# Kernel tuning notes

Measured on AMD Instinct MI355X. Metric: run time of the kernel, lower is better.

The kernel has to match this reference:

```python
import jax, jax.numpy as jnp
import numpy as np


def _pair_indices(n_beads):
    # Replicates the torch loop ordering: all pairs at offset 1, then offset 2, ...
    i_list, j_list = [], []
    for off in range(1, n_beads):
        i = np.arange(n_beads - off)
        i_list.append(i)
        j_list.append(i + off)
    return np.concatenate(i_list), np.concatenate(j_list)


def setup_inputs() -> dict:
    key = jax.random.key(0)
    data = jax.random.normal(key, (4096, 128, 3), dtype=jnp.float32)
    return {"data": data}


def _features(data):
    n = data.shape[1]
    i_idx, j_idx = _pair_indices(n)  # static numpy index arrays

    # All pairwise distances, ordered by bead offset (matches torch loop order)
    dvec = data[:, j_idx, :] - data[:, i_idx, :]          # [B, P, 3]
    distances = jnp.linalg.norm(dvec, axis=2)             # [B, P]

    # Adjacent bond vectors: x[j+1] - x[j]
    adj = data[:, 1:, :] - data[:, :-1, :]                # [B, n-1, 3]

    # Planar angles over consecutive bond-vector pairs
    a0, a1 = adj[:, : n - 2, :], adj[:, 1 : n - 1, :]
    angles = jnp.arccos(
        jnp.sum(a0 * a1, axis=2)
        / jnp.linalg.norm(a0, axis=2)
        / jnp.linalg.norm(a1, axis=2)
    )                                                     # [B, n-2]

    # Dihedrals
    cpa = jnp.cross(a0, a1, axis=2)                       # [B, n-2, 3]
    plane = jnp.cross(cpa[:, 1 : n - 2, :], adj[:, 1 : n - 2, :], axis=2)  # [B, n-3, 3]
    c0, c1 = cpa[:, : n - 3, :], cpa[:, 1 : n - 2, :]
    nc0 = jnp.linalg.norm(c0, axis=2)
    dihedral_cos = jnp.sum(c0 * c1, axis=2) / nc0 / jnp.linalg.norm(c1, axis=2)
    p0 = plane[:, : n - 3, :]
    dihedral_sin = jnp.sum(c0 * p0, axis=2) / nc0 / jnp.linalg.norm(p0, axis=2)

    return jnp.concatenate([distances, angles, dihedral_cos, dihedral_sin], axis=1)


def reference(data):
    return _features(data)
```

## Files before the change

kernel.cpp:

```cpp
#include <hip/hip_runtime.h>
#include <math.h>

constexpr int NB    = 128;
constexpr int NPAIR = NB * (NB - 1) / 2;
constexpr int NANG  = NB - 2;
constexpr int NDIH  = NB - 3;
constexpr int ROW   = NPAIR + NANG + 2 * NDIH;

__global__ __launch_bounds__(128, 8) void dist_kernel(
        const float* __restrict__ data, float* __restrict__ out) {
    __shared__ float4 s4[NB];
    const int b = blockIdx.x;
    const int t = threadIdx.x;
    const float* src = data + (size_t)b * (NB * 3);

    s4[t] = make_float4(src[3 * t], src[3 * t + 1], src[3 * t + 2], 0.0f);
    __syncthreads();

    float* orow = out + (size_t)b * ROW;

    float px[4], py[4], pz[4];
    #pragma unroll
    for (int k = 0; k < 4; ++k) {
        int idx = t - k; if (idx < 0) idx = 0;
        float4 v = s4[idx];
        px[k] = v.x; py[k] = v.y; pz[k] = v.z;
    }

    int base = 0;
    #pragma unroll 2
    for (int off = 1; off < NB; off += 4) {
        const int len = NB - off;
        int bk0 = base;
        int bk1 = bk0 + len;
        int bk2 = bk1 + len - 1;
        int bk3 = bk2 + len - 2;
        base    = bk3 + len - 3;
        if (t < len) {
            float4 pj = s4[t + off];
            float dx, dy, dz, d;
            dx = pj.x - px[0]; dy = pj.y - py[0]; dz = pj.z - pz[0];
            d = __builtin_amdgcn_sqrtf(dx*dx + dy*dy + dz*dz);
            orow[bk0 + t] = d;
            dx = pj.x - px[1]; dy = pj.y - py[1]; dz = pj.z - pz[1];
            d = __builtin_amdgcn_sqrtf(dx*dx + dy*dy + dz*dz);
            if (t >= 1) orow[bk1 + t - 1] = d;
            dx = pj.x - px[2]; dy = pj.y - py[2]; dz = pj.z - pz[2];
            d = __builtin_amdgcn_sqrtf(dx*dx + dy*dy + dz*dz);
            if (t >= 2) orow[bk2 + t - 2] = d;
            dx = pj.x - px[3]; dy = pj.y - py[3]; dz = pj.z - pz[3];
            d = __builtin_amdgcn_sqrtf(dx*dx + dy*dy + dz*dz);
            if (t >= 3) orow[bk3 + t - 3] = d;
        }
    }
}

__global__ __launch_bounds__(128) void angle_kernel(
        const float* __restrict__ data, float* __restrict__ out) {
    __shared__ float4 s4[NB];
    const int b = blockIdx.x;
    const int t = threadIdx.x;
    const float* src = data + (size_t)b * (NB * 3);

    s4[t] = make_float4(src[3 * t], src[3 * t + 1], src[3 * t + 2], 0.0f);
    __syncthreads();

    float* orow = out + (size_t)b * ROW;

    for (int v = t; v < NANG + 2 * NDIH; v += 128) {
        if (v < NANG) {
            int k = v;
            float4 p0 = s4[k], p1 = s4[k + 1], p2 = s4[k + 2];
            float a0x = p1.x - p0.x, a0y = p1.y - p0.y, a0z = p1.z - p0.z;
            float a1x = p2.x - p1.x, a1y = p2.y - p1.y, a1z = p2.z - p1.z;
            float d  = a0x * a1x + a0y * a1y + a0z * a1z;
            float r0 = rsqrtf(a0x * a0x + a0y * a0y + a0z * a0z);
            float r1 = rsqrtf(a1x * a1x + a1y * a1y + a1z * a1z);
            float c  = d * r0 * r1;
            c = fminf(1.0f, fmaxf(-1.0f, c));
            orow[NPAIR + k] = acosf(c);
        } else {
            int k = (v < NANG + NDIH) ? (v - NANG) : (v - NANG - NDIH);
            float4 p0 = s4[k], p1 = s4[k + 1], p2 = s4[k + 2], p3 = s4[k + 3];
            float e0x = p1.x - p0.x, e0y = p1.y - p0.y, e0z = p1.z - p0.z;
            float e1x = p2.x - p1.x, e1y = p2.y - p1.y, e1z = p2.z - p1.z;
            float e2x = p3.x - p2.x, e2y = p3.y - p2.y, e2z = p3.z - p2.z;
            float c0x = e0y * e1z - e0z * e1y;
            float c0y = e0z * e1x - e0x * e1z;
            float c0z = e0x * e1y - e0y * e1x;
            float c1x = e1y * e2z - e1z * e2y;
            float c1y = e1z * e2x - e1x * e2z;
            float c1z = e1x * e2y - e1y * e2x;
            float rn0 = rsqrtf(c0x * c0x + c0y * c0y + c0z * c0z);
            if (v < NANG + NDIH) {
                float d   = c0x * c1x + c0y * c1y + c0z * c1z;
                float rn1 = rsqrtf(c1x * c1x + c1y * c1y + c1z * c1z);
                orow[NPAIR + NANG + k] = d * rn0 * rn1;
            } else {
                float qx = c1y * e1z - c1z * e1y;
                float qy = c1z * e1x - c1x * e1z;
                float qz = c1x * e1y - c1y * e1x;
                float d  = c0x * qx + c0y * qy + c0z * qz;
                float rp = rsqrtf(qx * qx + qy * qy + qz * qz);
                orow[NPAIR + NANG + NDIH + k] = d * rn0 * rp;
            }
        }
    }
}

extern "C" void kernel_launch(void* const* d_in, const int* in_sizes, int n_in,
                              void* d_out, int out_size, void* d_ws, size_t ws_size,
                              hipStream_t stream) {
    const float* data = (const float*)d_in[0];
    float* out = (float*)d_out;
    const int batch = in_sizes[0] / (NB * 3);
    dist_kernel<<<batch, 128, 0, stream>>>(data, out);
    angle_kernel<<<batch, 128, 0, stream>>>(data, out);
}
```

Measured before the change: 37.20 us.

## Fuse distance and angle kernels into one persistent-style kernel over 4 batches

Merges the pairwise-distance kernel and the angle/dihedral kernel into a single launch, so the input is loaded into shared memory once per batch and one kernel launch is removed. Each block now loops over 4 batch elements strided by the grid size, with syncthreads guarding reuse of the shared buffer. The grid shrinks to a quarter of the batch count, which cuts per-block setup but reduces the number of blocks available to hide latency. The angle work now runs serially after the distance work within each block.

Result: slower. 43.15 us (+16.0%).

```diff
diff --git a/kernel.cpp b/kernel.cpp
--- a/kernel.cpp
+++ b/kernel.cpp
@@ -6,103 +6,96 @@
 constexpr int NANG  = NB - 2;
 constexpr int NDIH  = NB - 3;
 constexpr int ROW   = NPAIR + NANG + 2 * NDIH;
+constexpr int PP    = 4;
 
-__global__ __launch_bounds__(128, 8) void dist_kernel(
-        const float* __restrict__ data, float* __restrict__ out) {
+__global__ __launch_bounds__(128, 8) void protein_feat_kernel(
+        const float* __restrict__ data, float* __restrict__ out, int batch) {
     __shared__ float4 s4[NB];
-    const int b = blockIdx.x;
     const int t = threadIdx.x;
-    const float* src = data + (size_t)b * (NB * 3);
 
-    s4[t] = make_float4(src[3 * t], src[3 * t + 1], src[3 * t + 2], 0.0f);
-    __syncthreads();
+    for (int k = 0; k < PP; ++k) {
+        const int p = blockIdx.x + gridDim.x * k;
+        if (p >= batch) break;
 
-    float* orow = out + (size_t)b * ROW;
+        __syncthreads();
+        const float* src = data + (size_t)p * (NB * 3);
+        s4[t] = make_float4(src[3 * t], src[3 * t + 1], src[3 * t + 2], 0.0f);
+        __syncthreads();
 
-    float px[4], py[4], pz[4];
-    #pragma unroll
-    for (int k = 0; k < 4; ++k) {
-        int idx = t - k; if (idx < 0) idx = 0;
-        float4 v = s4[idx];
-        px[k] = v.x; py[k] = v.y; pz[k] = v.z;
-    }
+        float* orow = out + (size_t)p * ROW;
 
-    int base = 0;
-    #pragma unroll 2
-    for (int off = 1; off < NB; off += 4) {
-        const int len = NB - off;
-        int bk0 = base;
-        int bk1 = bk0 + len;
-        int bk2 = bk1 + len - 1;
-        int bk3 = bk2 + len - 2;
-        base    = bk3 + len - 3;
-        if (t < len) {
-            float4 pj = s4[t + off];
-            float dx, dy, dz, d;
-            dx = pj.x - px[0]; dy = pj.y - py[0]; dz = pj.z - pz[0];
-            d = __builtin_amdgcn_sqrtf(dx*dx + dy*dy + dz*dz);
-            orow[bk0 + t] = d;
-            dx = pj.x - px[1]; dy = pj.y - py[1]; dz = pj.z - pz[1];
-            d = __builtin_amdgcn_sqrtf(dx*dx + dy*dy + dz*dz);
-            if (t >= 1) orow[bk1 + t - 1] = d;
-            dx = pj.x - px[2]; dy = pj.y - py[2]; dz = pj.z - pz[2];
-            d = __builtin_amdgcn_sqrtf(dx*dx + dy*dy + dz*dz);
-            if (t >= 2) orow[bk2 + t - 2] = d;
-            dx = pj.x - px[3]; dy = pj.y - py[3]; dz = pj.z - pz[3];
-            d = __builtin_amdgcn_sqrtf(dx*dx + dy*dy + dz*dz);
-            if (t >= 3) orow[bk3 + t - 3] = d;
+        float px[4], py[4], pz[4];
+        #pragma unroll
+        for (int q = 0; q < 4; ++q) {
+            int idx = t - q; if (idx < 0) idx = 0;
+            float4 v = s4[idx];
+            px[q] = v.x; py[q] = v.y; pz[q] = v.z;
         }
-    }
-}
 
-__global__ __launch_bounds__(128) void angle_kernel(
-        const float* __restrict__ data, float* __restrict__ out) {
-    __shared__ float4 s4[NB];
-    const int b = blockIdx.x;
-    const int t = threadIdx.x;
-    const float* src = data + (size_t)b * (NB * 3);
+        int base = 0;
+        #pragma unroll 2
+        for (int off = 1; off < NB; off += 4) {
+            const int len = NB - off;
+            int bk0 = base;
+            int bk1 = bk0 + len;
+            int bk2 = bk1 + len - 1;
+            int bk3 = bk2 + len - 2;
+            base    = bk3 + len - 3;
+            if (t < len) {
+                float4 pj = s4[t + off];
+                float dx, dy, dz, d;
+                dx = pj.x - px[0]; dy = pj.y - py[0]; dz = pj.z - pz[0];
+                d = __builtin_amdgcn_sqrtf(dx*dx + dy*dy + dz*dz);
+                orow[bk0 + t] = d;
+                dx = pj.x - px[1]; dy = pj.y - py[1]; dz = pj.z - pz[1];
+                d = __builtin_amdgcn_sqrtf(dx*dx + dy*dy + dz*dz);
+                if (t >= 1) orow[bk1 + t - 1] = d;
+                dx = pj.x - px[2]; dy = pj.y - py[2]; dz = pj.z - pz[2];
+                d = __builtin_amdgcn_sqrtf(dx*dx + dy*dy + dz*dz);
+                if (t >= 2) orow[bk2 + t - 2] = d;
+                dx = pj.x - px[3]; dy = pj.y - py[3]; dz = pj.z - pz[3];
+                d = __builtin_amdgcn_sqrtf(dx*dx + dy*dy + dz*dz);
+                if (t >= 3) orow[bk3 + t - 3] = d;
+            }
+        }
 
-    s4[t] = make_float4(src[3 * t], src[3 * t + 1], src[3 * t + 2], 0.0f);
-    __syncthreads();
-
-    float* orow = out + (size_t)b * ROW;
-
-    for (int v = t; v < NANG + 2 * NDIH; v += 128) {
-        if (v < NANG) {
-            int k = v;
-            float4 p0 = s4[k], p1 = s4[k + 1], p2 = s4[k + 2];
-            float a0x = p1.x - p0.x, a0y = p1.y - p0.y, a0z = p1.z - p0.z;
-            float a1x = p2.x - p1.x, a1y = p2.y - p1.y, a1z = p2.z - p1.z;
-            float d  = a0x * a1x + a0y * a1y + a0z * a1z;
-            float r0 = rsqrtf(a0x * a0x + a0y * a0y + a0z * a0z);
-            float r1 = rsqrtf(a1x * a1x + a1y * a1y + a1z * a1z);
-            float c  = d * r0 * r1;
-            c = fminf(1.0f, fmaxf(-1.0f, c));
-            orow[NPAIR + k] = acosf(c);
-        } else {
-            int k = (v < NANG + NDIH) ? (v - NANG) : (v - NANG - NDIH);
-            float4 p0 = s4[k], p1 = s4[k + 1], p2 = s4[k + 2], p3 = s4[k + 3];
-            float e0x = p1.x - p0.x, e0y = p1.y - p0.y, e0z = p1.z - p0.z;
-            float e1x = p2.x - p1.x, e1y = p2.y - p1.y, e1z = p2.z - p1.z;
-            float e2x = p3.x - p2.x, e2y = p3.y - p2.y, e2z = p3.z - p2.z;
-            float c0x = e0y * e1z - e0z * e1y;
-            float c0y = e0z * e1x - e0x * e1z;
-            float c0z = e0x * e1y - e0y * e1x;
-            float c1x = e1y * e2z - e1z * e2y;
-            float c1y = e1z * e2x - e1x * e2z;
-            float c1z = e1x * e2y - e1y * e2x;
-            float rn0 = rsqrtf(c0x * c0x + c0y * c0y + c0z * c0z);
-            if (v < NANG + NDIH) {
-                float d   = c0x * c1x + c0y * c1y + c0z * c1z;
-                float rn1 = rsqrtf(c1x * c1x + c1y * c1y + c1z * c1z);
-                orow[NPAIR + NANG + k] = d * rn0 * rn1;
+        for (int v = t; v < NANG + 2 * NDIH; v += 128) {
+            if (v < NANG) {
+                int a = v;
+                float4 p0 = s4[a], p1 = s4[a + 1], p2 = s4[a + 2];
+                float a0x = p1.x - p0.x, a0y = p1.y - p0.y, a0z = p1.z - p0.z;
+                float a1x = p2.x - p1.x, a1y = p2.y - p1.y, a1z = p2.z - p1.z;
+                float d  = a0x * a1x + a0y * a1y + a0z * a1z;
+                float r0 = rsqrtf(a0x * a0x + a0y * a0y + a0z * a0z);
+                float r1 = rsqrtf(a1x * a1x + a1y * a1y + a1z * a1z);
+                float c  = d * r0 * r1;
+                c = fminf(1.0f, fmaxf(-1.0f, c));
+                orow[NPAIR + a] = acosf(c);
             } else {
-                float qx = c1y * e1z - c1z * e1y;
-                float qy = c1z * e1x - c1x * e1z;
-                float qz = c1x * e1y - c1y * e1x;
-                float d  = c0x * qx + c0y * qy + c0z * qz;
-                float rp = rsqrtf(qx * qx + qy * qy + qz * qz);
-                orow[NPAIR + NANG + NDIH + k] = d * rn0 * rp;
+                int a = (v < NANG + NDIH) ? (v - NANG) : (v - NANG - NDIH);
+                float4 p0 = s4[a], p1 = s4[a + 1], p2 = s4[a + 2], p3 = s4[a + 3];
+                float e0x = p1.x - p0.x, e0y = p1.y - p0.y, e0z = p1.z - p0.z;
+                float e1x = p2.x - p1.x, e1y = p2.y - p1.y, e1z = p2.z - p1.z;
+                float e2x = p3.x - p2.x, e2y = p3.y - p2.y, e2z = p3.z - p2.z;
+                float c0x = e0y * e1z - e0z * e1y;
+                float c0y = e0z * e1x - e0x * e1z;
+                float c0z = e0x * e1y - e0y * e1x;
+                float c1x = e1y * e2z - e1z * e2y;
+                float c1y = e1z * e2x - e1x * e2z;
+                float c1z = e1x * e2y - e1y * e2x;
+                float rn0 = rsqrtf(c0x * c0x + c0y * c0y + c0z * c0z);
+                if (v < NANG + NDIH) {
+                    float d   = c0x * c1x + c0y * c1y + c0z * c1z;
+                    float rn1 = rsqrtf(c1x * c1x + c1y * c1y + c1z * c1z);
+                    orow[NPAIR + NANG + a] = d * rn0 * rn1;
+                } else {
+                    float qx = c1y * e1z - c1z * e1y;
+                    float qy = c1z * e1x - c1x * e1z;
+                    float qz = c1x * e1y - c1y * e1x;
+                    float d  = c0x * qx + c0y * qy + c0z * qz;
+                    float rp = rsqrtf(qx * qx + qy * qy + qz * qz);
+                    orow[NPAIR + NANG + NDIH + a] = d * rn0 * rp;
+                }
             }
         }
     }
@@ -114,6 +107,6 @@
     const float* data = (const float*)d_in[0];
     float* out = (float*)d_out;
     const int batch = in_sizes[0] / (NB * 3);
-    dist_kernel<<<batch, 128, 0, stream>>>(data, out);
-    angle_kernel<<<batch, 128, 0, stream>>>(data, out);
+    const int grid  = (batch + PP - 1) / PP;
+    protein_feat_kernel<<<grid, 128, 0, stream>>>(data, out, batch);
 }
```
